# Kernel optimization log

Hardware: AMD Instinct MI355X
Metric: run time of the kernel (lower is better)

## Reference

```python
import jax, jax.numpy as jnp
import numpy as np

N_NODES = 50000
N_EDGES = 800000
IN_FEATS = 128
NUM_HEADS = 4
OUT_FEATS = 32


def setup_inputs() -> dict:
    key = jax.random.key(0)
    k1, k2, k3, k4 = jax.random.split(key, 4)
    feat = jax.random.normal(k1, (N_NODES, IN_FEATS), dtype=jnp.float32)
    # nn.Linear weight: [out_features, in_features] = [H*D, in]
    W = jax.random.normal(k2, (NUM_HEADS * OUT_FEATS, IN_FEATS), dtype=jnp.float32) * (1.0 / np.sqrt(IN_FEATS))
    src = jax.random.randint(k3, (N_EDGES,), 0, N_NODES, dtype=jnp.int32)
    dst = jax.random.randint(k4, (N_EDGES,), 0, N_NODES, dtype=jnp.int32)
    return {"feat": feat, "W": W, "src": src, "dst": dst}


def reference(feat, W, src, dst):
    N = feat.shape[0]
    H, D = NUM_HEADS, OUT_FEATS
    scale = jnp.float32(1.0 / np.sqrt(D))
    # fc: feat @ W.T  ->  [N, H, D]
    ft = (feat @ W.T).reshape(N, H, D)
    ft_src = ft[src]                                   # [E, H, D] gather
    # u_dot_v: per-edge, per-head dot product, scaled by sqrt(out_feats)
    a = jnp.einsum('ehd,ehd->eh', ft_src, ft[dst]) * scale  # [E, H]
    # edge softmax normalized by destination node (numerically stable)
    m = jax.ops.segment_max(a, dst, num_segments=N)    # [N, H]
    e = jnp.exp(a - m[dst])                            # [E, H]
    s = jax.ops.segment_sum(e, dst, num_segments=N)    # [N, H]
    sa = e / s[dst]                                    # [E, H]
    # u_mul_e + sum aggregation: scatter-add weighted source features into dst
    out = jax.ops.segment_sum(ft_src * sa[:, :, None], dst, num_segments=N)  # [N, H, D]
    return out
```

## Files before the change

### kernel.cpp

```cpp
#include <hip/hip_runtime.h>
#include <math.h>

#define NN 50000
#define NE 800000
#define HH 4
#define DD 32

typedef __attribute__((ext_vector_type(8))) short short8;
typedef __attribute__((ext_vector_type(4))) float f32x4;

__device__ __forceinline__ unsigned short f2bf(float x) {
    unsigned u = __float_as_uint(x);
    unsigned r = (u + 0x7FFF + ((u >> 16) & 1)) >> 16;
    return (unsigned short)r;
}

__device__ __forceinline__ short8 pack8(float4 p, float4 q) {
    short8 r;
    r[0] = (short)f2bf(p.x); r[1] = (short)f2bf(p.y);
    r[2] = (short)f2bf(p.z); r[3] = (short)f2bf(p.w);
    r[4] = (short)f2bf(q.x); r[5] = (short)f2bf(q.y);
    r[6] = (short)f2bf(q.z); r[7] = (short)f2bf(q.w);
    return r;
}

__global__ __launch_bounds__(256) void k_gemm(const float* __restrict__ feat,
                                              const float* __restrict__ W,
                                              float* __restrict__ ft, int N) {
    __shared__ short8 wlds[2048];

    int tid = threadIdx.x;
#pragma unroll
    for (int j = 0; j < 8; ++j) {
        int f = tid + j * 256;
        int kc = f >> 9, ct = (f >> 6) & 7, l = f & 63;
        int o = ct * 16 + (l & 15);
        int kb = kc * 32 + ((l >> 4) << 3);
        const float* wp = W + o * 128 + kb;
        float4 p = *(const float4*)wp;
        float4 q = *(const float4*)(wp + 4);
        wlds[f] = pack8(p, q);
    }
    __syncthreads();

    int l = tid & 63;
    int w = tid >> 6;
    int row0 = blockIdx.x * 64;
    int arow = row0 + w * 16 + (l & 15);
    bool valid = arow < N;
    const float* fb = feat + (size_t)(valid ? arow : 0) * 128 + ((l >> 4) << 3);

    f32x4 acc[8];
#pragma unroll
    for (int ct = 0; ct < 8; ++ct) acc[ct] = (f32x4){0.f, 0.f, 0.f, 0.f};

#pragma unroll
    for (int kc = 0; kc < 4; ++kc) {
        short8 a;
        if (valid) {
            float4 p = *(const float4*)(fb + kc * 32);
            float4 q = *(const float4*)(fb + kc * 32 + 4);
            a = pack8(p, q);
        } else {
            a = (short8){0, 0, 0, 0, 0, 0, 0, 0};
        }
#pragma unroll
        for (int ct = 0; ct < 8; ++ct) {
            short8 b = wlds[kc * 512 + ct * 64 + l];
            acc[ct] = __builtin_amdgcn_mfma_f32_16x16x32_bf16(a, b, acc[ct], 0, 0, 0);
        }
    }

    int oc = l & 15;
    int rg = l >> 4;
#pragma unroll
    for (int i = 0; i < 4; ++i) {
        int r = row0 + w * 16 + rg * 4 + i;
        if (r < N) {
            float* op = ft + (size_t)r * 128 + oc;
#pragma unroll
            for (int ct = 0; ct < 8; ++ct) op[ct * 16] = acc[ct][i];
        }
    }
}

__global__ __launch_bounds__(256) void k_rank(const int* __restrict__ dst,
                                              int* __restrict__ cnt,
                                              int* __restrict__ pos) {
    int e = blockIdx.x * 256 + threadIdx.x;
    if (e < NE) pos[e] = atomicAdd(&cnt[dst[e]], 1);
}

__global__ __launch_bounds__(256) void k_scan1(const int* __restrict__ cnt, int* __restrict__ row,
                                               int* __restrict__ partial, int n) {
    __shared__ int sh[256];
    int i = blockIdx.x * 256 + threadIdx.x;
    int x = (i < n) ? cnt[i] : 0;
    sh[threadIdx.x] = x;
    __syncthreads();
    for (int off = 1; off < 256; off <<= 1) {
        int v = (threadIdx.x >= off) ? sh[threadIdx.x - off] : 0;
        __syncthreads();
        sh[threadIdx.x] += v;
        __syncthreads();
    }
    if (i < n) row[i] = sh[threadIdx.x] - x;
    if (threadIdx.x == 255) partial[blockIdx.x] = sh[255];
}

__global__ __launch_bounds__(256) void k_scan2(int* __restrict__ partial, int nb) {
    __shared__ int sh[256];
    int t = threadIdx.x;
    int x = (t < nb) ? partial[t] : 0;
    sh[t] = x;
    __syncthreads();
    for (int off = 1; off < 256; off <<= 1) {
        int v = (t >= off) ? sh[t - off] : 0;
        __syncthreads();
        sh[t] += v;
        __syncthreads();
    }
    if (t < nb) partial[t] = sh[t] - x;
}

__global__ __launch_bounds__(256) void k_scan3(int* __restrict__ row,
                                               const int* __restrict__ partial, int n) {
    int i = blockIdx.x * 256 + threadIdx.x;
    if (i < n) row[i] += partial[blockIdx.x];
    if (i == 0) row[n] = NE;
}

__global__ __launch_bounds__(256) void k_fill(const int* __restrict__ src, const int* __restrict__ dst,
                                              const int* __restrict__ row, const int* __restrict__ pos,
                                              int* __restrict__ srcs) {
    int e = blockIdx.x * 256 + threadIdx.x;
    if (e >= NE) return;
    srcs[row[dst[e]] + pos[e]] = src[e];
}

__global__ __launch_bounds__(256) void k_agg(const float2* __restrict__ ft2,
                                             const int* __restrict__ row,
                                             const int* __restrict__ srcs,
                                             float2* __restrict__ out2) {
    int n = blockIdx.x * 4 + (threadIdx.x >> 6);
    int l = threadIdx.x & 63;
    int r0 = row[n], r1 = row[n + 1];
    size_t base = (size_t)n * 64 + l;
    float2 fd = ft2[base];
    float m = -INFINITY, s = 0.f;
    float ax = 0.f, ay = 0.f;
    int p = r0;
    for (; p + 1 < r1; p += 2) {
        int s0 = srcs[p], s1 = srcs[p + 1];
        float2 f0 = ft2[(size_t)s0 * 64 + l];
        float2 f1 = ft2[(size_t)s1 * 64 + l];
        float v0 = fd.x * f0.x + fd.y * f0.y;
        float v1 = fd.x * f1.x + fd.y * f1.y;
        v0 += __shfl_xor(v0, 1);  v1 += __shfl_xor(v1, 1);
        v0 += __shfl_xor(v0, 2);  v1 += __shfl_xor(v1, 2);
        v0 += __shfl_xor(v0, 4);  v1 += __shfl_xor(v1, 4);
        v0 += __shfl_xor(v0, 8);  v1 += __shfl_xor(v1, 8);
        v0 *= 0.17677669529663687f;
        v1 *= 0.17677669529663687f;
        float mn = fmaxf(fmaxf(m, v0), v1);
        float sc = __expf(m - mn);
        float w0 = __expf(v0 - mn);
        float w1 = __expf(v1 - mn);
        s = s * sc + w0 + w1;
        ax = ax * sc + w0 * f0.x + w1 * f1.x;
        ay = ay * sc + w0 * f0.y + w1 * f1.y;
        m = mn;
    }
    if (p < r1) {
        int s0 = srcs[p];
        float2 f0 = ft2[(size_t)s0 * 64 + l];
        float v0 = fd.x * f0.x + fd.y * f0.y;
        v0 += __shfl_xor(v0, 1);
        v0 += __shfl_xor(v0, 2);
        v0 += __shfl_xor(v0, 4);
        v0 += __shfl_xor(v0, 8);
        v0 *= 0.17677669529663687f;
        float mn = fmaxf(m, v0);
        float sc = __expf(m - mn);
        float w0 = __expf(v0 - mn);
        s = s * sc + w0;
        ax = ax * sc + w0 * f0.x;
        ay = ay * sc + w0 * f0.y;
    }
    float inv = (r1 > r0) ? 1.f / s : 0.f;
    out2[base] = make_float2(ax * inv, ay * inv);
}

extern "C" void kernel_launch(void* const* d_in, const int* in_sizes, int n_in,
                              void* d_out, int out_size, void* d_ws, size_t ws_size,
                              hipStream_t stream) {
    const float* feat = (const float*)d_in[0];
    const float* W    = (const float*)d_in[1];
    const int*   src  = (const int*)d_in[2];
    const int*   dst  = (const int*)d_in[3];
    float* out = (float*)d_out;

    float* ft   = (float*)d_ws;
    int*   row  = (int*)(ft + (size_t)NN * 128);
    int*   pos  = row + (NN + 1);
    int*   srcs = pos + NE;
    int*   cnt  = srcs + NE;
    int*   part = cnt + NN;

    const int NB1 = (NN + 255) / 256;

    hipMemsetAsync(cnt, 0, (size_t)NN * sizeof(int), stream);
    k_rank<<<(NE + 255) / 256, 256, 0, stream>>>(dst, cnt, pos);
    k_scan1<<<NB1, 256, 0, stream>>>(cnt, row, part, NN);
    k_scan2<<<1, 256, 0, stream>>>(part, NB1);
    k_scan3<<<NB1, 256, 0, stream>>>(row, part, NN);
    k_fill<<<(NE + 255) / 256, 256, 0, stream>>>(src, dst, row, pos, srcs);

    k_gemm<<<(NN + 63) / 64, 256, 0, stream>>>(feat, W, ft, NN);
    k_agg<<<NN / 4, 256, 0, stream>>>((const float2*)ft, row, srcs, (float2*)out);
}
```

Baseline: 221.3 us.

## Store projected features as bf16 and fuse edge ranking into GEMM kernel

```diff
diff --git a/kernel.cpp b/kernel.cpp
--- a/kernel.cpp
+++ b/kernel.cpp
@@ -24,9 +24,15 @@
     return r;
 }
 
+__device__ __forceinline__ float bflo(unsigned u) { return __uint_as_float(u << 16); }
+__device__ __forceinline__ float bfhi(unsigned u) { return __uint_as_float(u & 0xFFFF0000u); }
+
 __global__ __launch_bounds__(256) void k_gemm(const float* __restrict__ feat,
                                               const float* __restrict__ W,
-                                              float* __restrict__ ft, int N) {
+                                              unsigned short* __restrict__ ft, int N,
+                                              const int* __restrict__ dst,
+                                              int* __restrict__ cnt,
+                                              int* __restrict__ pos) {
     __shared__ short8 wlds[2048];
 
     int tid = threadIdx.x;
@@ -77,18 +83,15 @@
     for (int i = 0; i < 4; ++i) {
         int r = row0 + w * 16 + rg * 4 + i;
         if (r < N) {
-            float* op = ft + (size_t)r * 128 + oc;
-#pragma unroll
-            for (int ct = 0; ct < 8; ++ct) op[ct * 16] = acc[ct][i];
+            unsigned short* op = ft + (size_t)r * 128 + oc;
+#pragma unroll
+            for (int ct = 0; ct < 8; ++ct) op[ct * 16] = f2bf(acc[ct][i]);
         }
     }
-}
-
-__global__ __launch_bounds__(256) void k_rank(const int* __restrict__ dst,
-                                              int* __restrict__ cnt,
-                                              int* __restrict__ pos) {
-    int e = blockIdx.x * 256 + threadIdx.x;
-    if (e < NE) pos[e] = atomicAdd(&cnt[dst[e]], 1);
+
+    int nthr = gridDim.x * 256;
+    for (int e = blockIdx.x * 256 + tid; e < NE; e += nthr)
+        pos[e] = atomicAdd(&cnt[dst[e]], 1);
 }
 
 __global__ __launch_bounds__(256) void k_scan1(const int* __restrict__ cnt, int* __restrict__ row,
@@ -138,7 +141,7 @@
     srcs[row[dst[e]] + pos[e]] = src[e];
 }
 
-__global__ __launch_bounds__(256) void k_agg(const float2* __restrict__ ft2,
+__global__ __launch_bounds__(256) void k_agg(const unsigned* __restrict__ ftb,
                                              const int* __restrict__ row,
                                              const int* __restrict__ srcs,
                                              float2* __restrict__ out2) {
@@ -146,16 +149,19 @@
     int l = threadIdx.x & 63;
     int r0 = row[n], r1 = row[n + 1];
     size_t base = (size_t)n * 64 + l;
-    float2 fd = ft2[base];
+    unsigned ud = ftb[base];
+    float fdx = bflo(ud), fdy = bfhi(ud);
     float m = -INFINITY, s = 0.f;
     float ax = 0.f, ay = 0.f;
     int p = r0;
     for (; p + 1 < r1; p += 2) {
         int s0 = srcs[p], s1 = srcs[p + 1];
-        float2 f0 = ft2[(size_t)s0 * 64 + l];
-        float2 f1 = ft2[(size_t)s1 * 64 + l];
-        float v0 = fd.x * f0.x + fd.y * f0.y;
-        float v1 = fd.x * f1.x + fd.y * f1.y;
+        unsigned u0 = ftb[(size_t)s0 * 64 + l];
+        unsigned u1 = ftb[(size_t)s1 * 64 + l];
+        float f0x = bflo(u0), f0y = bfhi(u0);
+        float f1x = bflo(u1), f1y = bfhi(u1);
+        float v0 = fdx * f0x + fdy * f0y;
+        float v1 = fdx * f1x + fdy * f1y;
         v0 += __shfl_xor(v0, 1);  v1 += __shfl_xor(v1, 1);
         v0 += __shfl_xor(v0, 2);  v1 += __shfl_xor(v1, 2);
         v0 += __shfl_xor(v0, 4);  v1 += __shfl_xor(v1, 4);
@@ -167,14 +173,15 @@
         float w0 = __expf(v0 - mn);
         float w1 = __expf(v1 - mn);
         s = s * sc + w0 + w1;
-        ax = ax * sc + w0 * f0.x + w1 * f1.x;
-        ay = ay * sc + w0 * f0.y + w1 * f1.y;
+        ax = ax * sc + w0 * f0x + w1 * f1x;
+        ay = ay * sc + w0 * f0y + w1 * f1y;
         m = mn;
     }
     if (p < r1) {
         int s0 = srcs[p];
-        float2 f0 = ft2[(size_t)s0 * 64 + l];
-        float v0 = fd.x * f0.x + fd.y * f0.y;
+        unsigned u0 = ftb[(size_t)s0 * 64 + l];
+        float f0x = bflo(u0), f0y = bfhi(u0);
+        float v0 = fdx * f0x + fdy * f0y;
         v0 += __shfl_xor(v0, 1);
         v0 += __shfl_xor(v0, 2);
         v0 += __shfl_xor(v0, 4);
@@ -184,8 +191,8 @@
         float sc = __expf(m - mn);
         float w0 = __expf(v0 - mn);
         s = s * sc + w0;
-        ax = ax * sc + w0 * f0.x;
-        ay = ay * sc + w0 * f0.y;
+        ax = ax * sc + w0 * f0x;
+        ay = ay * sc + w0 * f0y;
     }
     float inv = (r1 > r0) ? 1.f / s : 0.f;
     out2[base] = make_float2(ax * inv, ay * inv);
@@ -200,22 +207,20 @@
     const int*   dst  = (const int*)d_in[3];
     float* out = (float*)d_out;
 
-    float* ft   = (float*)d_ws;
-    int*   row  = (int*)(ft + (size_t)NN * 128);
-    int*   pos  = row + (NN + 1);
-    int*   srcs = pos + NE;
-    int*   cnt  = srcs + NE;
-    int*   part = cnt + NN;
+    unsigned short* ft = (unsigned short*)d_ws;
+    int* row  = (int*)(ft + (size_t)NN * 128);
+    int* pos  = row + (NN + 1);
+    int* srcs = pos + NE;
+    int* cnt  = srcs + NE;
+    int* part = cnt + NN;
 
     const int NB1 = (NN + 255) / 256;
 
     hipMemsetAsync(cnt, 0, (size_t)NN * sizeof(int), stream);
-    k_rank<<<(NE + 255) / 256, 256, 0, stream>>>(dst, cnt, pos);
+    k_gemm<<<(NN + 63) / 64, 256, 0, stream>>>(feat, W, ft, NN, dst, cnt, pos);
     k_scan1<<<NB1, 256, 0, stream>>>(cnt, row, part, NN);
     k_scan2<<<1, 256, 0, stream>>>(part, NB1);
     k_scan3<<<NB1, 256, 0, stream>>>(row, part, NN);
     k_fill<<<(NE + 255) / 256, 256, 0, stream>>>(src, dst, row, pos, srcs);
-
-    k_gemm<<<(NN + 63) / 64, 256, 0, stream>>>(feat, W, ft, NN);
-    k_agg<<<NN / 4, 256, 0, stream>>>((const float2*)ft, row, srcs, (float2*)out);
-}
+    k_agg<<<NN / 4, 256, 0, stream>>>((const unsigned*)ft, row, srcs, (float2*)out);
+}
```

Measured after the change: 211.4 us. 1.05x faster.
